# Optimization experiments

Hardware: AMD Instinct MI355X
Metric: run time of the kernel (lower is better)

Reference implementation:

```python
import jax, jax.numpy as jnp
import numpy as np

NUM_USER, BATCH, NUM_NT = 8, 16384, 128
T = 0.3  # SE threshold from the original module


def setup_inputs() -> dict:
    key = jax.random.key(0)
    k1, k2 = jax.random.split(key)
    h = jax.random.normal(k1, (NUM_USER, BATCH, NUM_NT), dtype=jnp.float32)
    v = jax.random.normal(k2, (NUM_USER, BATCH, NUM_NT), dtype=jnp.float32)
    N = jnp.ones((), dtype=jnp.float32)
    return {"h": h, "v": v, "N": N}


def reference(h, v, N):
    num_user, batch, num_nt = h.shape
    d = num_nt // 2
    # split real/imag halves into complex views
    h_c = jax.lax.complex(h[..., :d], h[..., d:])  # (user, batch, d)
    v_c = jax.lax.complex(v[..., :d], v[..., d:])  # (user, batch, d)
    # per-sample Frobenius norm over (user, d) and power scaling to sqrt(num_user)
    norms = jnp.sqrt(jnp.sum(jnp.real(v_c) ** 2 + jnp.imag(v_c) ** 2, axis=(0, 2)))  # (batch,)
    scale = jnp.sqrt(jnp.float32(num_user)) / norms
    v_scaled = v_c * scale[None, :, None]
    # signal: diag(h_user @ v_user^H) per sample == row-wise complex dot, with SCALED v
    S = jnp.abs(jnp.sum(h_c * jnp.conj(v_scaled), axis=-1)) ** 2  # (user, batch)
    # interference: original uses UNSCALED v[j] (faithful to source)
    A = jnp.einsum('ibt,jbt->ijb', h_c, jnp.conj(v_c))  # (user_i, user_j, batch)
    Iall = jnp.abs(A) ** 2
    Ip = jnp.sum(Iall, axis=1) - jnp.einsum('iib->ib', Iall)  # exclude j == i
    SINR = S / (Ip + N)
    R_user = jnp.log2(1.0 + SINR)  # (user, batch)
    R_per_user_p = jnp.mean(R_user, axis=1)  # (user,)
    # Rp = sum_i ( -R_user_i + 10^(T - R_user_i) ) per sample
    Rp = jnp.sum(10.0 ** (T - R_user) - R_user, axis=0)  # (batch,)
    return jnp.mean(Rp), R_per_user_p, jnp.sum(R_per_user_p)
```

## Files before the change

### kernel.cpp

```cpp
#include <hip/hip_runtime.h>
#include <hip/hip_bf16.h>


typedef float v2f __attribute__((ext_vector_type(2)));
typedef _Float16 h2  __attribute__((ext_vector_type(2)));
typedef _Float16 h4  __attribute__((ext_vector_type(4)));

struct alignas(16) h2x4 { h2 a, b, c, d; };

constexpr int U_    = 8;
constexpr int B_    = 16384;
constexpr int NT_   = 128;
constexpr int ROWH_ = 136;
constexpr int WPB_  = 4;
constexpr int NBLK_MAX = 4096;
constexpr float T_THRESH = 0.3f;
constexpr float LOG2_10  = 3.3219280948873623f;

__device__ __forceinline__ float hw_log2(float x) { return __builtin_amdgcn_logf(x); }
__device__ __forceinline__ float hw_exp2(float x) { return __builtin_amdgcn_exp2f(x); }

__global__ __launch_bounds__(256, 4) void se_main(const float* __restrict__ h,
                                                  const float* __restrict__ vv,
                                                  const float* __restrict__ Np,
                                                  float* __restrict__ partial) {
    __shared__ alignas(16) _Float16 lds[WPB_][2][U_ * ROWH_];
    __shared__ float red_f[WPB_];
    __shared__ float red_R[WPB_][U_];

    const int tid  = threadIdx.x;
    const int wave = tid >> 6;
    const int lane = tid & 63;
    const int ui   = lane >> 3;
    const int uj   = lane & 7;
    const float Nval = Np[0];

    _Float16* hb = lds[wave][0];
    _Float16* vb = lds[wave][1];

    float lane_sumR = 0.0f;
    float lane_sumf = 0.0f;

    const int gwave = blockIdx.x * WPB_ + wave;
    const int totw  = gridDim.x * WPB_;

    for (int b = gwave; b < B_; b += totw) {
        v2f nsq2 = {0.0f, 0.0f};
        #pragma unroll
        for (int t = 0; t < 4; ++t) {
            const int idx = t * 64 + lane;
            const int row = idx >> 5;
            const int c4  = idx & 31;
            const size_t goff = (size_t)row * ((size_t)B_ * NT_) + (size_t)b * NT_ + (size_t)c4 * 4;
            const float4 h4f = *reinterpret_cast<const float4*>(h  + goff);
            const float4 v4f = *reinterpret_cast<const float4*>(vv + goff);
            const v2f va = {v4f.x, v4f.y}, vbp = {v4f.z, v4f.w};
            nsq2 = __builtin_elementwise_fma(va,  va,  nsq2);
            nsq2 = __builtin_elementwise_fma(vbp, vbp, nsq2);
            h4 hh = { (_Float16)h4f.x, (_Float16)h4f.y, (_Float16)h4f.z, (_Float16)h4f.w };
            h4 vh = { (_Float16)v4f.x, (_Float16)v4f.y, (_Float16)v4f.z, (_Float16)v4f.w };
            *reinterpret_cast<h4*>(&hb[row * ROWH_ + c4 * 4]) = hh;
            *reinterpret_cast<h4*>(&vb[row * ROWH_ + c4 * 4]) = vh;
        }
        float nsq = nsq2[0] + nsq2[1];

        float t1 = 0.0f, t2 = 0.0f, t3 = 0.0f, t4 = 0.0f;
        const _Float16* hrow = &hb[ui * ROWH_];
        const _Float16* vrow = &vb[uj * ROWH_];
        #pragma unroll
        for (int c = 0; c < 8; ++c) {
            const h2x4 hre = *reinterpret_cast<const h2x4*>(hrow + c * 8);
            const h2x4 him = *reinterpret_cast<const h2x4*>(hrow + 64 + c * 8);
            const h2x4 vre = *reinterpret_cast<const h2x4*>(vrow + c * 8);
            const h2x4 vim = *reinterpret_cast<const h2x4*>(vrow + 64 + c * 8);
            t1 = __builtin_amdgcn_fdot2(hre.a, vre.a, t1, false);
            t2 = __builtin_amdgcn_fdot2(him.a, vim.a, t2, false);
            t3 = __builtin_amdgcn_fdot2(him.a, vre.a, t3, false);
            t4 = __builtin_amdgcn_fdot2(hre.a, vim.a, t4, false);
            t1 = __builtin_amdgcn_fdot2(hre.b, vre.b, t1, false);
            t2 = __builtin_amdgcn_fdot2(him.b, vim.b, t2, false);
            t3 = __builtin_amdgcn_fdot2(him.b, vre.b, t3, false);
            t4 = __builtin_amdgcn_fdot2(hre.b, vim.b, t4, false);
            t1 = __builtin_amdgcn_fdot2(hre.c, vre.c, t1, false);
            t2 = __builtin_amdgcn_fdot2(him.c, vim.c, t2, false);
            t3 = __builtin_amdgcn_fdot2(him.c, vre.c, t3, false);
            t4 = __builtin_amdgcn_fdot2(hre.c, vim.c, t4, false);
            t1 = __builtin_amdgcn_fdot2(hre.d, vre.d, t1, false);
            t2 = __builtin_amdgcn_fdot2(him.d, vim.d, t2, false);
            t3 = __builtin_amdgcn_fdot2(him.d, vre.d, t3, false);
            t4 = __builtin_amdgcn_fdot2(hre.d, vim.d, t4, false);
        }
        const float are  = t1 + t2;
        const float aim  = t3 - t4;
        const float Iall = are * are + aim * aim;

        const float diag = __shfl(Iall, ui * 9, 64);
        float rowsum = Iall;
        rowsum += __shfl_xor(rowsum, 1, 64);  nsq += __shfl_xor(nsq, 1, 64);
        rowsum += __shfl_xor(rowsum, 2, 64);  nsq += __shfl_xor(nsq, 2, 64);
        rowsum += __shfl_xor(rowsum, 4, 64);  nsq += __shfl_xor(nsq, 4, 64);
        nsq += __shfl_xor(nsq, 8,  64);
        nsq += __shfl_xor(nsq, 16, 64);
        nsq += __shfl_xor(nsq, 32, 64);

        const float Ip   = rowsum - diag;
        const float S    = (8.0f / nsq) * diag;
        const float SINR = S / (Ip + Nval);
        const float R    = hw_log2(1.0f + SINR);

        lane_sumR += R;
        lane_sumf += hw_exp2((T_THRESH - R) * LOG2_10) - R;
    }

    float wf = lane_sumf;
    #pragma unroll
    for (int m = 1; m < 64; m <<= 1) wf += __shfl_xor(wf, m, 64);
    wf *= 0.125f;
    if (lane == 0) red_f[wave] = wf;
    if (uj == 0)   red_R[wave][ui] = lane_sumR;
    __syncthreads();

    if (tid < U_) {
        float s = 0.0f;
        #pragma unroll
        for (int w = 0; w < WPB_; ++w) s += red_R[w][tid];
        partial[blockIdx.x * 9 + 1 + tid] = s;
    } else if (tid == U_) {
        float s = 0.0f;
        #pragma unroll
        for (int w = 0; w < WPB_; ++w) s += red_f[w];
        partial[blockIdx.x * 9] = s;
    }
}

__global__ __launch_bounds__(256) void se_final(const float* __restrict__ partial,
                                                float* __restrict__ out, int nblk) {
    __shared__ float sums[9];
    if (threadIdx.x < 9) sums[threadIdx.x] = 0.0f;
    __syncthreads();

    float local[9];
    #pragma unroll
    for (int s = 0; s < 9; ++s) local[s] = 0.0f;
    for (int b = threadIdx.x; b < nblk; b += 256) {
        #pragma unroll
        for (int s = 0; s < 9; ++s) local[s] += partial[b * 9 + s];
    }
    #pragma unroll
    for (int s = 0; s < 9; ++s) atomicAdd(&sums[s], local[s]);
    __syncthreads();

    if (threadIdx.x == 0) {
        const float inv = 1.0f / (float)B_;
        out[0] = sums[0] * inv;
        float tot = 0.0f;
        #pragma unroll
        for (int i = 0; i < U_; ++i) {
            const float r = sums[1 + i] * inv;
            out[1 + i] = r;
            tot += r;
        }
        out[9] = tot;
    }
}

extern "C" void kernel_launch(void* const* d_in, const int* in_sizes, int n_in,
                              void* d_out, int out_size, void* d_ws, size_t ws_size,
                              hipStream_t stream) {
    const float* h  = (const float*)d_in[0];
    const float* v  = (const float*)d_in[1];
    const float* Np = (const float*)d_in[2];
    float* out      = (float*)d_out;
    float* partial  = (float*)d_ws;

    int nblk = NBLK_MAX;
    const size_t need = (size_t)NBLK_MAX * 9 * sizeof(float);
    if (ws_size < need) {
        nblk = (int)(ws_size / (9 * sizeof(float)));
        if (nblk < 1) nblk = 1;
    }

    se_main<<<nblk, 256, 0, stream>>>(h, v, Np, partial);
    se_final<<<1, 256, 0, stream>>>(partial, out, nblk);
}
```

Baseline: 172.1 us.

## Software-pipeline global loads with double-buffered LDS tiles per wave

Each wave now processes a fixed block of four samples, prefetching the next sample's h and v rows into registers while the current sample's dot products run from a double-buffered LDS tile. The grid shrinks to 1024 blocks, and launch bounds relax to 2 blocks per SM to leave room for the extra registers. The aim is to hide global memory latency behind compute. The cost is higher register and LDS use, lower occupancy, and no fallback when the workspace is smaller than the fixed block count needs.

Result: no change. 173.4 us (+0.7%).

```diff
diff --git a/kernel.cpp b/kernel.cpp
--- a/kernel.cpp
+++ b/kernel.cpp
@@ -3,8 +3,8 @@
 
 
 typedef float v2f __attribute__((ext_vector_type(2)));
-typedef _Float16 h2  __attribute__((ext_vector_type(2)));
-typedef _Float16 h4  __attribute__((ext_vector_type(4)));
+typedef _Float16 h2 __attribute__((ext_vector_type(2)));
+typedef _Float16 h4 __attribute__((ext_vector_type(4)));
 
 struct alignas(16) h2x4 { h2 a, b, c, d; };
 
@@ -13,18 +13,47 @@
 constexpr int NT_   = 128;
 constexpr int ROWH_ = 136;
 constexpr int WPB_  = 4;
-constexpr int NBLK_MAX = 4096;
+constexpr int SPW_  = 4;
+constexpr int NBLK_ = 1024;
 constexpr float T_THRESH = 0.3f;
 constexpr float LOG2_10  = 3.3219280948873623f;
 
 __device__ __forceinline__ float hw_log2(float x) { return __builtin_amdgcn_logf(x); }
 __device__ __forceinline__ float hw_exp2(float x) { return __builtin_amdgcn_exp2f(x); }
 
-__global__ __launch_bounds__(256, 4) void se_main(const float* __restrict__ h,
+__device__ __forceinline__ void load_sample(const float* __restrict__ h,
+                                            const float* __restrict__ v,
+                                            int b, int lane, float4* hr, float4* vr) {
+    #pragma unroll
+    for (int t = 0; t < 4; ++t) {
+        const int idx = t * 64 + lane;
+        const int row = idx >> 5;
+        const int c4  = idx & 31;
+        const size_t goff = (size_t)row * ((size_t)B_ * NT_) + (size_t)b * NT_ + (size_t)c4 * 4;
+        hr[t] = *reinterpret_cast<const float4*>(h + goff);
+        vr[t] = *reinterpret_cast<const float4*>(v + goff);
+    }
+}
+
+__device__ __forceinline__ void store_tile(_Float16* hb, _Float16* vb, int lane,
+                                           const float4* hr, const float4* vr) {
+    #pragma unroll
+    for (int t = 0; t < 4; ++t) {
+        const int idx = t * 64 + lane;
+        const int row = idx >> 5;
+        const int c4  = idx & 31;
+        h4 hh = { (_Float16)hr[t].x, (_Float16)hr[t].y, (_Float16)hr[t].z, (_Float16)hr[t].w };
+        h4 vh = { (_Float16)vr[t].x, (_Float16)vr[t].y, (_Float16)vr[t].z, (_Float16)vr[t].w };
+        *reinterpret_cast<h4*>(&hb[row * ROWH_ + c4 * 4]) = hh;
+        *reinterpret_cast<h4*>(&vb[row * ROWH_ + c4 * 4]) = vh;
+    }
+}
+
+__global__ __launch_bounds__(256, 2) void se_main(const float* __restrict__ h,
                                                   const float* __restrict__ vv,
                                                   const float* __restrict__ Np,
                                                   float* __restrict__ partial) {
-    __shared__ alignas(16) _Float16 lds[WPB_][2][U_ * ROWH_];
+    __shared__ alignas(16) _Float16 tiles[WPB_][2][2][U_ * ROWH_];
     __shared__ float red_f[WPB_];
     __shared__ float red_R[WPB_][U_];
 
@@ -35,34 +64,38 @@
     const int uj   = lane & 7;
     const float Nval = Np[0];
 
-    _Float16* hb = lds[wave][0];
-    _Float16* vb = lds[wave][1];
-
     float lane_sumR = 0.0f;
     float lane_sumf = 0.0f;
 
-    const int gwave = blockIdx.x * WPB_ + wave;
-    const int totw  = gridDim.x * WPB_;
-
-    for (int b = gwave; b < B_; b += totw) {
+    const int base = blockIdx.x * (WPB_ * SPW_) + wave * SPW_;
+
+    float4 ph[4], pv[4];
+    load_sample(h, vv, base, lane, ph, pv);
+
+    #pragma unroll
+    for (int s = 0; s < SPW_; ++s) {
+        _Float16* hb = tiles[wave][s & 1][0];
+        _Float16* vb = tiles[wave][s & 1][1];
+
+        store_tile(hb, vb, lane, ph, pv);
+
         v2f nsq2 = {0.0f, 0.0f};
         #pragma unroll
         for (int t = 0; t < 4; ++t) {
-            const int idx = t * 64 + lane;
-            const int row = idx >> 5;
-            const int c4  = idx & 31;
-            const size_t goff = (size_t)row * ((size_t)B_ * NT_) + (size_t)b * NT_ + (size_t)c4 * 4;
-            const float4 h4f = *reinterpret_cast<const float4*>(h  + goff);
-            const float4 v4f = *reinterpret_cast<const float4*>(vv + goff);
-            const v2f va = {v4f.x, v4f.y}, vbp = {v4f.z, v4f.w};
-            nsq2 = __builtin_elementwise_fma(va,  va,  nsq2);
-            nsq2 = __builtin_elementwise_fma(vbp, vbp, nsq2);
-            h4 hh = { (_Float16)h4f.x, (_Float16)h4f.y, (_Float16)h4f.z, (_Float16)h4f.w };
-            h4 vh = { (_Float16)v4f.x, (_Float16)v4f.y, (_Float16)v4f.z, (_Float16)v4f.w };
-            *reinterpret_cast<h4*>(&hb[row * ROWH_ + c4 * 4]) = hh;
-            *reinterpret_cast<h4*>(&vb[row * ROWH_ + c4 * 4]) = vh;
+            const v2f a = {pv[t].x, pv[t].y}, b2 = {pv[t].z, pv[t].w};
+            nsq2 = __builtin_elementwise_fma(a,  a,  nsq2);
+            nsq2 = __builtin_elementwise_fma(b2, b2, nsq2);
         }
         float nsq = nsq2[0] + nsq2[1];
+
+        if (s + 1 < SPW_) load_sample(h, vv, base + s + 1, lane, ph, pv);
+
+        nsq += __shfl_xor(nsq, 1,  64);
+        nsq += __shfl_xor(nsq, 2,  64);
+        nsq += __shfl_xor(nsq, 4,  64);
+        nsq += __shfl_xor(nsq, 8,  64);
+        nsq += __shfl_xor(nsq, 16, 64);
+        nsq += __shfl_xor(nsq, 32, 64);
 
         float t1 = 0.0f, t2 = 0.0f, t3 = 0.0f, t4 = 0.0f;
         const _Float16* hrow = &hb[ui * ROWH_];
@@ -96,12 +129,9 @@
 
         const float diag = __shfl(Iall, ui * 9, 64);
         float rowsum = Iall;
-        rowsum += __shfl_xor(rowsum, 1, 64);  nsq += __shfl_xor(nsq, 1, 64);
-        rowsum += __shfl_xor(rowsum, 2, 64);  nsq += __shfl_xor(nsq, 2, 64);
-        rowsum += __shfl_xor(rowsum, 4, 64);  nsq += __shfl_xor(nsq, 4, 64);
-        nsq += __shfl_xor(nsq, 8,  64);
-        nsq += __shfl_xor(nsq, 16, 64);
-        nsq += __shfl_xor(nsq, 32, 64);
+        rowsum += __shfl_xor(rowsum, 1, 64);
+        rowsum += __shfl_xor(rowsum, 2, 64);
+        rowsum += __shfl_xor(rowsum, 4, 64);
 
         const float Ip   = rowsum - diag;
         const float S    = (8.0f / nsq) * diag;
@@ -173,13 +203,6 @@
     float* out      = (float*)d_out;
     float* partial  = (float*)d_ws;
 
-    int nblk = NBLK_MAX;
-    const size_t need = (size_t)NBLK_MAX * 9 * sizeof(float);
-    if (ws_size < need) {
-        nblk = (int)(ws_size / (9 * sizeof(float)));
-        if (nblk < 1) nblk = 1;
-    }
-
-    se_main<<<nblk, 256, 0, stream>>>(h, v, Np, partial);
-    se_final<<<1, 256, 0, stream>>>(partial, out, nblk);
-}
+    se_main<<<NBLK_, 256, 0, stream>>>(h, v, Np, partial);
+    se_final<<<1, 256, 0, stream>>>(partial, out, NBLK_);
+}
```
